# Kernel tuning notes

Hardware: AMD Instinct MI355X
Metric: run time of the kernel (lower is better)

## Reference

```python
import jax, jax.numpy as jnp
import numpy as np

EMBED = 1024
B, I, J = 8, 2048, 2048
SCALE = EMBED ** -0.5


def setup_inputs() -> dict:
    key = jax.random.key(0)
    ks = jax.random.split(key, 5)
    s = EMBED ** -0.5  # init scale for weights
    return {
        "q_in": jax.random.normal(ks[0], (B, I, EMBED), dtype=jnp.float32),
        "k_v": jax.random.normal(ks[1], (B, J, EMBED), dtype=jnp.float32),
        "Wq": jax.random.normal(ks[2], (EMBED, EMBED), dtype=jnp.float32) * s,
        "bq": jnp.zeros((EMBED,), dtype=jnp.float32),
        "Wk": jax.random.normal(ks[3], (EMBED, EMBED), dtype=jnp.float32) * s,
        "bk": jnp.zeros((EMBED,), dtype=jnp.float32),
        "Wv": jax.random.normal(ks[4], (EMBED, EMBED), dtype=jnp.float32) * s,
        "bv": jnp.zeros((EMBED,), dtype=jnp.float32),
    }


def reference(q_in, k_v, Wq, bq, Wk, bk, Wv, bv):
    # Linear projections (torch Linear: x @ W.T + b; here W stored as [in, out])
    q = q_in @ Wq + bq            # [b, i, d]
    k = k_v @ Wk + bk             # [b, j, d]
    v = k_v @ Wv + bv             # [b, j, d]
    sim = jnp.einsum('bid,bjd->bij', q, k) * SCALE  # [b, i, j]
    attn = jax.nn.softmax(sim, axis=-1)
    # dropout with drop_rate=0.0 is identity
    out = jnp.einsum('bij,bjd->bid', attn, v)       # [b, i, d]
    return out
```

## Files before the change

### kernel.cpp

```cpp
#include <hip/hip_runtime.h>
#include <hip/hip_bf16.h>


#define BATCH 8
#define SEQ   2048
#define EMB   1024
#define SC2   0.045084222f

typedef __attribute__((ext_vector_type(8))) short bf16x8;
typedef __attribute__((ext_vector_type(4))) float f32x4;
typedef __attribute__((ext_vector_type(4))) unsigned short u16x4;
typedef __attribute__((ext_vector_type(8))) unsigned short u16x8;
typedef __attribute__((ext_vector_type(4))) float fl4;

__device__ __forceinline__ unsigned short f2bf(float f) {
    unsigned u = __builtin_bit_cast(unsigned, f);
    unsigned r = u + 0x7fffu + ((u >> 16) & 1u);
    return (unsigned short)(r >> 16);
}
__device__ __forceinline__ float bf2f(unsigned short s) {
    return __builtin_bit_cast(float, ((unsigned)s) << 16);
}
__device__ __forceinline__ void gload16(const unsigned short* g, unsigned short* l) {
    __builtin_amdgcn_global_load_lds(
        (const __attribute__((address_space(1))) void*)g,
        (__attribute__((address_space(3))) void*)l, 16, 0, 0);
}

__global__ __launch_bounds__(256)
void convert_all(const float* __restrict__ q_in, const float* __restrict__ k_v,
                 const float* __restrict__ Wq, const float* __restrict__ Wk,
                 const float* __restrict__ Wv,
                 unsigned short* __restrict__ qbin, unsigned short* __restrict__ kvbin,
                 unsigned short* __restrict__ Wt)
{
    const int bid = blockIdx.x;
    const int tid = threadIdx.x;
    if (bid < 4096) {
        const size_t N = (size_t)BATCH * SEQ * EMB;
        size_t idx = ((size_t)bid * 256 + tid) * 8;
        const size_t stride = (size_t)4096 * 256 * 8;
        for (; idx < N; idx += stride) {
            fl4 a0 = *(const fl4*)&q_in[idx];
            fl4 a1 = *(const fl4*)&q_in[idx + 4];
            fl4 b0 = *(const fl4*)&k_v[idx];
            fl4 b1 = *(const fl4*)&k_v[idx + 4];
            u16x8 ua, ub;
#pragma unroll
            for (int i = 0; i < 4; i++) {
                ua[i] = f2bf(a0[i]); ua[i + 4] = f2bf(a1[i]);
                ub[i] = f2bf(b0[i]); ub[i + 4] = f2bf(b1[i]);
            }
            *(u16x8*)&qbin[idx] = ua;
            *(u16x8*)&kvbin[idx] = ub;
        }
    } else {
        const int b2 = bid - 4096;
        const int wsel = b2 >> 8, rest = b2 & 255;
        const float* W = (wsel == 0) ? Wq : (wsel == 1) ? Wk : Wv;
        unsigned short* O = Wt + (size_t)wsel * EMB * EMB;
        const int k0 = (rest >> 4) * 64;
        const int n0 = (rest & 15) * 64;
        __shared__ unsigned short l[64 * 65];
#pragma unroll
        for (int it = 0; it < 16; it++) {
            const int lin = it * 256 + tid;
            const int k = lin >> 6, n = lin & 63;
            l[n * 65 + k] = f2bf(W[(size_t)(k0 + k) * EMB + n0 + n]);
        }
        __syncthreads();
#pragma unroll
        for (int it = 0; it < 16; it++) {
            const int lin = it * 256 + tid;
            const int n = lin >> 6, k = lin & 63;
            O[(size_t)(n0 + n) * EMB + k0 + k] = l[n * 65 + k];
        }
    }
}

__device__ __forceinline__ void stageT(const unsigned short* lanebase, size_t rstride,
                                       unsigned short* lwave) {
#pragma unroll
    for (int i = 0; i < 2; i++)
        gload16(lanebase + (size_t)(i * 128) * rstride, lwave + i * 4096);
}

#define PIPE_TILE(SLOT, DO_STAGE, STAGE_A_BASE, STAGE_A_LDS, STAGE_B_BASE, STAGE_B_LDS) \
    {                                                                           \
        const unsigned short* pa = &sA[SLOT][0];                                \
        const unsigned short* pb = &sB[SLOT][0];                                \
        bf16x8 a0 = *(bf16x8*)&pa[aoff0];                                       \
        bf16x8 a1 = *(bf16x8*)&pa[aoff0 + 512];                                 \
        bf16x8 a2 = *(bf16x8*)&pa[aoff0 + 1024];                                \
        bf16x8 a3 = *(bf16x8*)&pa[aoff0 + 1536];                                \
        bf16x8 a4 = *(bf16x8*)&pa[aoff0 + 2048];                                \
        bf16x8 a5 = *(bf16x8*)&pa[aoff0 + 2560];                                \
        bf16x8 a6 = *(bf16x8*)&pa[aoff0 + 3072];                                \
        bf16x8 a7 = *(bf16x8*)&pa[aoff0 + 3584];                                \
        bf16x8 bv0 = *(bf16x8*)&pb[boff0];                                      \
        bf16x8 bv1 = *(bf16x8*)&pb[boff0 + 512];                                \
        bf16x8 bv2 = *(bf16x8*)&pb[boff0 + 1024];                               \
        bf16x8 bv3 = *(bf16x8*)&pb[boff0 + 1536];                               \
        if (DO_STAGE) stageT(STAGE_A_BASE, strideA, STAGE_A_LDS);               \
        __builtin_amdgcn_s_setprio(1);                                          \
        acc[0][0] = __builtin_amdgcn_mfma_f32_16x16x32_bf16(a0, bv0, acc[0][0], 0, 0, 0); \
        acc[0][1] = __builtin_amdgcn_mfma_f32_16x16x32_bf16(a0, bv1, acc[0][1], 0, 0, 0); \
        acc[0][2] = __builtin_amdgcn_mfma_f32_16x16x32_bf16(a0, bv2, acc[0][2], 0, 0, 0); \
        acc[0][3] = __builtin_amdgcn_mfma_f32_16x16x32_bf16(a0, bv3, acc[0][3], 0, 0, 0); \
        acc[1][0] = __builtin_amdgcn_mfma_f32_16x16x32_bf16(a1, bv0, acc[1][0], 0, 0, 0); \
        acc[1][1] = __builtin_amdgcn_mfma_f32_16x16x32_bf16(a1, bv1, acc[1][1], 0, 0, 0); \
        acc[1][2] = __builtin_amdgcn_mfma_f32_16x16x32_bf16(a1, bv2, acc[1][2], 0, 0, 0); \
        acc[1][3] = __builtin_amdgcn_mfma_f32_16x16x32_bf16(a1, bv3, acc[1][3], 0, 0, 0); \
        acc[2][0] = __builtin_amdgcn_mfma_f32_16x16x32_bf16(a2, bv0, acc[2][0], 0, 0, 0); \
        acc[2][1] = __builtin_amdgcn_mfma_f32_16x16x32_bf16(a2, bv1, acc[2][1], 0, 0, 0); \
        acc[2][2] = __builtin_amdgcn_mfma_f32_16x16x32_bf16(a2, bv2, acc[2][2], 0, 0, 0); \
        acc[2][3] = __builtin_amdgcn_mfma_f32_16x16x32_bf16(a2, bv3, acc[2][3], 0, 0, 0); \
        acc[3][0] = __builtin_amdgcn_mfma_f32_16x16x32_bf16(a3, bv0, acc[3][0], 0, 0, 0); \
        acc[3][1] = __builtin_amdgcn_mfma_f32_16x16x32_bf16(a3, bv1, acc[3][1], 0, 0, 0); \
        acc[3][2] = __builtin_amdgcn_mfma_f32_16x16x32_bf16(a3, bv2, acc[3][2], 0, 0, 0); \
        acc[3][3] = __builtin_amdgcn_mfma_f32_16x16x32_bf16(a3, bv3, acc[3][3], 0, 0, 0); \
        __builtin_amdgcn_s_setprio(0);                                          \
        if (DO_STAGE) stageT(STAGE_B_BASE, strideB, STAGE_B_LDS);               \
        __builtin_amdgcn_s_setprio(1);                                          \
        acc[4][0] = __builtin_amdgcn_mfma_f32_16x16x32_bf16(a4, bv0, acc[4][0], 0, 0, 0); \
        acc[4][1] = __builtin_amdgcn_mfma_f32_16x16x32_bf16(a4, bv1, acc[4][1], 0, 0, 0); \
        acc[4][2] = __builtin_amdgcn_mfma_f32_16x16x32_bf16(a4, bv2, acc[4][2], 0, 0, 0); \
        acc[4][3] = __builtin_amdgcn_mfma_f32_16x16x32_bf16(a4, bv3, acc[4][3], 0, 0, 0); \
        acc[5][0] = __builtin_amdgcn_mfma_f32_16x16x32_bf16(a5, bv0, acc[5][0], 0, 0, 0); \
        acc[5][1] = __builtin_amdgcn_mfma_f32_16x16x32_bf16(a5, bv1, acc[5][1], 0, 0, 0); \
        acc[5][2] = __builtin_amdgcn_mfma_f32_16x16x32_bf16(a5, bv2, acc[5][2], 0, 0, 0); \
        acc[5][3] = __builtin_amdgcn_mfma_f32_16x16x32_bf16(a5, bv3, acc[5][3], 0, 0, 0); \
        acc[6][0] = __builtin_amdgcn_mfma_f32_16x16x32_bf16(a6, bv0, acc[6][0], 0, 0, 0); \
        acc[6][1] = __builtin_amdgcn_mfma_f32_16x16x32_bf16(a6, bv1, acc[6][1], 0, 0, 0); \
        acc[6][2] = __builtin_amdgcn_mfma_f32_16x16x32_bf16(a6, bv2, acc[6][2], 0, 0, 0); \
        acc[6][3] = __builtin_amdgcn_mfma_f32_16x16x32_bf16(a6, bv3, acc[6][3], 0, 0, 0); \
        acc[7][0] = __builtin_amdgcn_mfma_f32_16x16x32_bf16(a7, bv0, acc[7][0], 0, 0, 0); \
        acc[7][1] = __builtin_amdgcn_mfma_f32_16x16x32_bf16(a7, bv1, acc[7][1], 0, 0, 0); \
        acc[7][2] = __builtin_amdgcn_mfma_f32_16x16x32_bf16(a7, bv2, acc[7][2], 0, 0, 0); \
        acc[7][3] = __builtin_amdgcn_mfma_f32_16x16x32_bf16(a7, bv3, acc[7][3], 0, 0, 0); \
        __builtin_amdgcn_s_setprio(0);                                          \
        asm volatile("s_waitcnt vmcnt(4)" ::: "memory");                        \
        __builtin_amdgcn_s_barrier();                                           \
        __builtin_amdgcn_sched_barrier(0);                                      \
    }

__device__ __forceinline__ void pipe_gemm(
    const unsigned short* __restrict__ Asrc,
    const unsigned short* __restrict__ Bsrc,
    const size_t strideA, const size_t strideB, const int NT,
    unsigned short (*sA)[8192], unsigned short (*sB)[8192],
    const int lwave, const int aoff0, const int boff0,
    f32x4 acc[8][4])
{
    stageT(Asrc, strideA, &sA[0][lwave]);
    stageT(Bsrc, strideB, &sB[0][lwave]);
    stageT(Asrc + 32, strideA, &sA[1][lwave]);
    stageT(Bsrc + 32, strideB, &sB[1][lwave]);
    asm volatile("s_waitcnt vmcnt(4)" ::: "memory");
    __builtin_amdgcn_s_barrier();
    __builtin_amdgcn_sched_barrier(0);

    for (int T = 0; T < NT; ++T) {
        const int s = T & 3;
        const int doStage = (T + 2 < NT);
        const int s2 = (T + 2) & 3;
        PIPE_TILE(s, doStage, Asrc + (T + 2) * 32, &sA[s2][lwave],
                  Bsrc + (T + 2) * 32, &sB[s2][lwave]);
    }
}

#define PIPE_PREAMBLE                                                     \
    __shared__ unsigned short sMem[65536];                    \
    unsigned short (*sA)[8192] = (unsigned short (*)[8192])sMem;          \
    unsigned short (*sB)[8192] = (unsigned short (*)[8192])(sMem + 32768);\
    const int tid = threadIdx.x, lane = tid & 63;                         \
    const int wid = tid >> 6, wr = wid >> 2, wn = wid & 3;                \
    const int r = lane & 15, g = lane >> 4;                               \
    const int lwave = (wid << 9);                                         \
    const int scol = ((tid & 3) ^ ((tid >> 3) & 3)) * 8;                  \
    const int gsw = (g ^ ((r >> 1) & 3)) * 8;                             \
    const int aoff0 = (wr * 128 + r) * 32 + gsw;                          \
    const int boff0 = (wn * 64 + r) * 32 + gsw;                           \
    f32x4 acc[8][4];                                                      \
    _Pragma("unroll") for (int i_ = 0; i_ < 8; i_++)                      \
    _Pragma("unroll") for (int j_ = 0; j_ < 4; j_++) acc[i_][j_] = (f32x4)0.0f;

__device__ __forceinline__ void lds_flush_bf16(const unsigned short* sP,
                                               unsigned short* gbase,
                                               size_t gstride, int tid)
{
    const int lane = tid & 63, wv = tid >> 6;
    const int rowsel = lane >> 5, jj = lane & 31;
#pragma unroll
    for (int it = 0; it < 16; ++it) {
        const int row = it * 16 + wv * 2 + rowsel;
        const int byte = row * 512 + ((jj * 16) ^ ((row & 7) << 4));
        u16x8 v = *(const u16x8*)((const char*)sP + byte);
        *(u16x8*)&gbase[(size_t)row * gstride + jj * 8] = v;
    }
}

__global__ __launch_bounds__(512, 1)
void proj_all(const unsigned short* __restrict__ Wt,
              const unsigned short* __restrict__ qbin,
              const unsigned short* __restrict__ kvbin,
              const float* __restrict__ bq, const float* __restrict__ bk,
              const float* __restrict__ bv,
              unsigned short* __restrict__ qb, unsigned short* __restrict__ kb,
              unsigned short* __restrict__ vt)
{
    PIPE_PREAMBLE
    const int bid = blockIdx.x;
    const size_t strideA = EMB, strideB = EMB;
    const unsigned short* Asrc;
    const unsigned short* Bsrc;
    int d0 = 0, i0 = 0, m0 = 0, n0 = 0;
    const bool qrole = (bid < 256);
    if (qrole) {
        const int lid = (bid & 7) * 32 + (bid >> 3);
        d0 = (lid & 3) * 256; i0 = (lid >> 2) * 256;
        Asrc = Wt + (size_t)(d0 + (tid >> 2)) * EMB + scol;
        Bsrc = qbin + (size_t)(i0 + (tid >> 2)) * EMB + scol;
    } else {
        const int b2 = bid - 256;
        const int lid = (b2 & 7) * 64 + (b2 >> 3);
        n0 = (lid & 7) * 256; m0 = (lid >> 3) * 256;
        Asrc = kvbin + (size_t)(m0 + (tid >> 2)) * EMB + scol;
        Bsrc = Wt + (size_t)EMB * EMB + (size_t)(n0 + (tid >> 2)) * EMB + scol;
    }

    pipe_gemm(Asrc, Bsrc, strideA, strideB, EMB / 32, sA, sB, lwave, aoff0, boff0, acc);

    if (qrole) {
#pragma unroll
        for (int mm = 0; mm < 8; mm++) {
            const int colb = wr * 128 + mm * 16 + g * 4;
            const fl4 b4 = *(const fl4*)&bq[d0 + colb];
#pragma unroll
            for (int n = 0; n < 4; n++) {
                const int row = wn * 64 + n * 16 + r;
                u16x4 u;
#pragma unroll
                for (int c = 0; c < 4; c++) u[c] = f2bf(acc[mm][n][c] + b4[c]);
                const int byte = row * 512 + ((colb * 2) ^ ((row & 7) << 4));
                *(u16x4*)((char*)sMem + byte) = u;
            }
        }
        __syncthreads();
        lds_flush_bf16(sMem, qb + (size_t)i0 * EMB + d0, EMB, tid);
    } else {
        const int b = m0 >> 11;
        const int j0l = m0 & 2047;
        if (n0 < 1024) {
#pragma unroll
            for (int mm = 0; mm < 8; mm++) {
                const int ibase = m0 + wr * 128 + mm * 16 + g * 4;
#pragma unroll
                for (int n = 0; n < 4; n++) {
                    const int col = n0 + wn * 64 + n * 16 + r;
                    const float bb = bk[col];
#pragma unroll
                    for (int c = 0; c < 4; c++)
                        kb[(size_t)(ibase + c) * EMB + col] = f2bf(acc[mm][n][c] + bb);
                }
            }
        } else {
#pragma unroll
            for (int mm = 0; mm < 8; mm++) {
                const int colb = wr * 128 + mm * 16 + g * 4;
#pragma unroll
                for (int n = 0; n < 4; n++) {
                    const int row = wn * 64 + n * 16 + r;
                    const float bb = bv[n0 - 1024 + row];
                    u16x4 u;
#pragma unroll
                    for (int c = 0; c < 4; c++) u[c] = f2bf(acc[mm][n][c] + bb);
                    const int byte = row * 512 + ((colb * 2) ^ ((row & 7) << 4));
                    *(u16x4*)((char*)sMem + byte) = u;
                }
            }
            __syncthreads();
            lds_flush_bf16(sMem, vt + ((size_t)b * EMB + (n0 - 1024)) * SEQ + j0l,
                           SEQ, tid);
        }
    }
}

__global__ __launch_bounds__(512, 1)
void qk256_kernel(const unsigned short* __restrict__ qb,
                  const unsigned short* __restrict__ kb,
                  unsigned short* __restrict__ P,
                  float* __restrict__ Ppart)
{
    PIPE_PREAMBLE
    const int bid = blockIdx.x;
    const int lid = (bid & 7) * 64 + (bid >> 3);
    const int b = lid >> 6, jt = (lid >> 3) & 7, it = lid & 7;
    const int j0 = jt * 256, i0 = it * 256;
    const size_t strideA = EMB, strideB = EMB;
    const unsigned short* Ag = kb + (size_t)b * SEQ * EMB;
    const unsigned short* Bg = qb + (size_t)b * SEQ * EMB;
    const unsigned short* Asrc = Ag + (size_t)(j0 + (tid >> 2)) * EMB + scol;
    const unsigned short* Bsrc = Bg + (size_t)(i0 + (tid >> 2)) * EMB + scol;

    pipe_gemm(Asrc, Bsrc, strideA, strideB, EMB / 32, sA, sB, lwave, aoff0, boff0, acc);

    float ps[4] = {0.f, 0.f, 0.f, 0.f};
#pragma unroll
    for (int mm = 0; mm < 8; mm++) {
        const int colb = wr * 128 + mm * 16 + g * 4;
#pragma unroll
        for (int n = 0; n < 4; n++) {
            const int row = wn * 64 + n * 16 + r;
            u16x4 u;
#pragma unroll
            for (int c = 0; c < 4; c++) {
                const float p = exp2f(acc[mm][n][c] * SC2);
                ps[n] += p;
                u[c] = f2bf(p);
            }
            const int byte = row * 512 + ((colb * 2) ^ ((row & 7) << 4));
            *(u16x4*)((char*)sMem + byte) = u;
        }
    }
#pragma unroll
    for (int n = 0; n < 4; n++) {
        ps[n] += __shfl_xor(ps[n], 16);
        ps[n] += __shfl_xor(ps[n], 32);
    }
    if (g == 0) {
        const int slot = jt * 2 + wr;
        float* pp = Ppart + (size_t)slot * (BATCH * SEQ) + (size_t)b * SEQ;
#pragma unroll
        for (int n = 0; n < 4; n++)
            pp[i0 + wn * 64 + n * 16 + r] = ps[n];
    }
    __syncthreads();
    unsigned short* Pb = P + (size_t)b * SEQ * SEQ;
    lds_flush_bf16(sMem, Pb + (size_t)i0 * SEQ + j0, SEQ, tid);
}

__global__ __launch_bounds__(512, 1)
void pv256_kernel(const unsigned short* __restrict__ P,
                  const unsigned short* __restrict__ vt,
                  const float* __restrict__ Ppart,
                  float* __restrict__ out)
{
    PIPE_PREAMBLE
    const int bid = blockIdx.x;
    const int lid = (bid & 7) * 32 + (bid >> 3);
    const int b = lid >> 5, it = (lid >> 2) & 7, dt = lid & 3;
    const int d0 = dt * 256, i0 = it * 256;
    const size_t strideA = SEQ, strideB = SEQ;
    const unsigned short* Ag = vt + (size_t)b * EMB * SEQ;
    const unsigned short* Bg = P + (size_t)b * SEQ * SEQ;
    const unsigned short* Asrc = Ag + (size_t)(d0 + (tid >> 2)) * SEQ + scol;
    const unsigned short* Bsrc = Bg + (size_t)(i0 + (tid >> 2)) * SEQ + scol;

    float inv[4];
#pragma unroll
    for (int n = 0; n < 4; n++) {
        const int row = b * SEQ + i0 + wn * 64 + n * 16 + r;
        float s = 0.f;
#pragma unroll
        for (int slot = 0; slot < 16; slot++)
            s += Ppart[(size_t)slot * (BATCH * SEQ) + row];
        inv[n] = 1.0f / s;
    }

    pipe_gemm(Asrc, Bsrc, strideA, strideB, SEQ / 32, sA, sB, lwave, aoff0, boff0, acc);

    float* ob = out + (size_t)b * SEQ * EMB;
    float* sF = (float*)sMem;
#pragma unroll
    for (int h = 0; h < 2; h++) {
        if (wr == h) {
#pragma unroll
            for (int mm = 0; mm < 8; mm++) {
                const int colb = mm * 16 + g * 4;
#pragma unroll
                for (int n = 0; n < 4; n++) {
                    const int row = wn * 64 + n * 16 + r;
                    fl4 o;
#pragma unroll
                    for (int c = 0; c < 4; c++) o[c] = acc[mm][n][c] * inv[n];
                    const int byte = row * 512 + ((colb * 4) ^ ((row & 7) << 4));
                    *(fl4*)((char*)sF + byte) = o;
                }
            }
        }
        __syncthreads();
        {
            const int rowsel = lane >> 5, jj = lane & 31;
#pragma unroll
            for (int itx = 0; itx < 16; ++itx) {
                const int row = itx * 16 + wid * 2 + rowsel;
                const int byte = row * 512 + ((jj * 16) ^ ((row & 7) << 4));
                fl4 v = *(const fl4*)((const char*)sF + byte);
                *(fl4*)&ob[(size_t)(i0 + row) * EMB + d0 + h * 128 + jj * 4] = v;
            }
        }
        if (h == 0) __syncthreads();
    }
}

extern "C" void kernel_launch(void* const* d_in, const int* in_sizes, int n_in,
                              void* d_out, int out_size, void* d_ws, size_t ws_size,
                              hipStream_t stream)
{
    const float* q_in = (const float*)d_in[0];
    const float* k_v  = (const float*)d_in[1];
    const float* Wq   = (const float*)d_in[2];
    const float* bq   = (const float*)d_in[3];
    const float* Wk   = (const float*)d_in[4];
    const float* bk   = (const float*)d_in[5];
    const float* Wv   = (const float*)d_in[6];
    const float* bv   = (const float*)d_in[7];
    float* out = (float*)d_out;

    char* ws = (char*)d_ws;
    unsigned short* qbin = (unsigned short*)(ws);
    unsigned short* kvbin= (unsigned short*)(ws + (size_t)33554432);
    unsigned short* P    = (unsigned short*)(ws);
    unsigned short* qb   = (unsigned short*)(ws + (size_t)67108864);
    unsigned short* kb   = (unsigned short*)(ws + (size_t)100663296);
    unsigned short* vt   = (unsigned short*)(ws + (size_t)134217728);
    unsigned short* Wt   = (unsigned short*)(ws + (size_t)167772160);
    float*          Ppart= (float*)(ws + (size_t)174063616);

    convert_all<<<4864, 256, 0, stream>>>(q_in, k_v, Wq, Wk, Wv, qbin, kvbin, Wt);
    proj_all<<<768, 512, 0, stream>>>(Wt, qbin, kvbin, bq, bk, bv, qb, kb, vt);
    qk256_kernel<<<512, 512, 0, stream>>>(qb, kb, P, Ppart);
    pv256_kernel<<<256, 512, 0, stream>>>(P, vt, Ppart, out);
}
```

Measured before the change: 293.9 us.

## Split GEMM main loop into barrier-synchronized half-phases with interleaved LDS reads

Adds a phased pipe_gemm variant in which each K-tile is split into two halves. Each half loads its A fragments from LDS, issues one global-to-LDS stage, hits a workgroup barrier and lgkmcnt wait, then runs 16 MFMAs, so waves stay in lockstep and LDS reads overlap more evenly with compute. The tail iterations now wait with vmcnt(0) when no new stage was issued. The QK and PV kernels switch to the new variant, which cuts register pressure for A fragments but adds extra barriers per tile.

Result: slower. 306.2 us (+4.2%).

```diff
diff --git a/kernel.cpp b/kernel.cpp
--- a/kernel.cpp
+++ b/kernel.cpp
@@ -85,64 +85,41 @@
         gload16(lanebase + (size_t)(i * 128) * rstride, lwave + i * 4096);
 }
 
-#define PIPE_TILE(SLOT, DO_STAGE, STAGE_A_BASE, STAGE_A_LDS, STAGE_B_BASE, STAGE_B_LDS) \
-    {                                                                           \
-        const unsigned short* pa = &sA[SLOT][0];                                \
-        const unsigned short* pb = &sB[SLOT][0];                                \
-        bf16x8 a0 = *(bf16x8*)&pa[aoff0];                                       \
-        bf16x8 a1 = *(bf16x8*)&pa[aoff0 + 512];                                 \
-        bf16x8 a2 = *(bf16x8*)&pa[aoff0 + 1024];                                \
-        bf16x8 a3 = *(bf16x8*)&pa[aoff0 + 1536];                                \
-        bf16x8 a4 = *(bf16x8*)&pa[aoff0 + 2048];                                \
-        bf16x8 a5 = *(bf16x8*)&pa[aoff0 + 2560];                                \
-        bf16x8 a6 = *(bf16x8*)&pa[aoff0 + 3072];                                \
-        bf16x8 a7 = *(bf16x8*)&pa[aoff0 + 3584];                                \
-        bf16x8 bv0 = *(bf16x8*)&pb[boff0];                                      \
-        bf16x8 bv1 = *(bf16x8*)&pb[boff0 + 512];                                \
-        bf16x8 bv2 = *(bf16x8*)&pb[boff0 + 1024];                               \
-        bf16x8 bv3 = *(bf16x8*)&pb[boff0 + 1536];                               \
-        if (DO_STAGE) stageT(STAGE_A_BASE, strideA, STAGE_A_LDS);               \
-        __builtin_amdgcn_s_setprio(1);                                          \
-        acc[0][0] = __builtin_amdgcn_mfma_f32_16x16x32_bf16(a0, bv0, acc[0][0], 0, 0, 0); \
-        acc[0][1] = __builtin_amdgcn_mfma_f32_16x16x32_bf16(a0, bv1, acc[0][1], 0, 0, 0); \
-        acc[0][2] = __builtin_amdgcn_mfma_f32_16x16x32_bf16(a0, bv2, acc[0][2], 0, 0, 0); \
-        acc[0][3] = __builtin_amdgcn_mfma_f32_16x16x32_bf16(a0, bv3, acc[0][3], 0, 0, 0); \
-        acc[1][0] = __builtin_amdgcn_mfma_f32_16x16x32_bf16(a1, bv0, acc[1][0], 0, 0, 0); \
-        acc[1][1] = __builtin_amdgcn_mfma_f32_16x16x32_bf16(a1, bv1, acc[1][1], 0, 0, 0); \
-        acc[1][2] = __builtin_amdgcn_mfma_f32_16x16x32_bf16(a1, bv2, acc[1][2], 0, 0, 0); \
-        acc[1][3] = __builtin_amdgcn_mfma_f32_16x16x32_bf16(a1, bv3, acc[1][3], 0, 0, 0); \
-        acc[2][0] = __builtin_amdgcn_mfma_f32_16x16x32_bf16(a2, bv0, acc[2][0], 0, 0, 0); \
-        acc[2][1] = __builtin_amdgcn_mfma_f32_16x16x32_bf16(a2, bv1, acc[2][1], 0, 0, 0); \
-        acc[2][2] = __builtin_amdgcn_mfma_f32_16x16x32_bf16(a2, bv2, acc[2][2], 0, 0, 0); \
-        acc[2][3] = __builtin_amdgcn_mfma_f32_16x16x32_bf16(a2, bv3, acc[2][3], 0, 0, 0); \
-        acc[3][0] = __builtin_amdgcn_mfma_f32_16x16x32_bf16(a3, bv0, acc[3][0], 0, 0, 0); \
-        acc[3][1] = __builtin_amdgcn_mfma_f32_16x16x32_bf16(a3, bv1, acc[3][1], 0, 0, 0); \
-        acc[3][2] = __builtin_amdgcn_mfma_f32_16x16x32_bf16(a3, bv2, acc[3][2], 0, 0, 0); \
-        acc[3][3] = __builtin_amdgcn_mfma_f32_16x16x32_bf16(a3, bv3, acc[3][3], 0, 0, 0); \
-        __builtin_amdgcn_s_setprio(0);                                          \
-        if (DO_STAGE) stageT(STAGE_B_BASE, strideB, STAGE_B_LDS);               \
-        __builtin_amdgcn_s_setprio(1);                                          \
-        acc[4][0] = __builtin_amdgcn_mfma_f32_16x16x32_bf16(a4, bv0, acc[4][0], 0, 0, 0); \
-        acc[4][1] = __builtin_amdgcn_mfma_f32_16x16x32_bf16(a4, bv1, acc[4][1], 0, 0, 0); \
-        acc[4][2] = __builtin_amdgcn_mfma_f32_16x16x32_bf16(a4, bv2, acc[4][2], 0, 0, 0); \
-        acc[4][3] = __builtin_amdgcn_mfma_f32_16x16x32_bf16(a4, bv3, acc[4][3], 0, 0, 0); \
-        acc[5][0] = __builtin_amdgcn_mfma_f32_16x16x32_bf16(a5, bv0, acc[5][0], 0, 0, 0); \
-        acc[5][1] = __builtin_amdgcn_mfma_f32_16x16x32_bf16(a5, bv1, acc[5][1], 0, 0, 0); \
-        acc[5][2] = __builtin_amdgcn_mfma_f32_16x16x32_bf16(a5, bv2, acc[5][2], 0, 0, 0); \
-        acc[5][3] = __builtin_amdgcn_mfma_f32_16x16x32_bf16(a5, bv3, acc[5][3], 0, 0, 0); \
-        acc[6][0] = __builtin_amdgcn_mfma_f32_16x16x32_bf16(a6, bv0, acc[6][0], 0, 0, 0); \
-        acc[6][1] = __builtin_amdgcn_mfma_f32_16x16x32_bf16(a6, bv1, acc[6][1], 0, 0, 0); \
-        acc[6][2] = __builtin_amdgcn_mfma_f32_16x16x32_bf16(a6, bv2, acc[6][2], 0, 0, 0); \
-        acc[6][3] = __builtin_amdgcn_mfma_f32_16x16x32_bf16(a6, bv3, acc[6][3], 0, 0, 0); \
-        acc[7][0] = __builtin_amdgcn_mfma_f32_16x16x32_bf16(a7, bv0, acc[7][0], 0, 0, 0); \
-        acc[7][1] = __builtin_amdgcn_mfma_f32_16x16x32_bf16(a7, bv1, acc[7][1], 0, 0, 0); \
-        acc[7][2] = __builtin_amdgcn_mfma_f32_16x16x32_bf16(a7, bv2, acc[7][2], 0, 0, 0); \
-        acc[7][3] = __builtin_amdgcn_mfma_f32_16x16x32_bf16(a7, bv3, acc[7][3], 0, 0, 0); \
-        __builtin_amdgcn_s_setprio(0);                                          \
-        asm volatile("s_waitcnt vmcnt(4)" ::: "memory");                        \
-        __builtin_amdgcn_s_barrier();                                           \
-        __builtin_amdgcn_sched_barrier(0);                                      \
-    }
+#define MFMA16_LO(A0,A1,A2,A3)                                                  \
+        acc[0][0] = __builtin_amdgcn_mfma_f32_16x16x32_bf16(A0, bv0, acc[0][0], 0, 0, 0); \
+        acc[0][1] = __builtin_amdgcn_mfma_f32_16x16x32_bf16(A0, bv1, acc[0][1], 0, 0, 0); \
+        acc[0][2] = __builtin_amdgcn_mfma_f32_16x16x32_bf16(A0, bv2, acc[0][2], 0, 0, 0); \
+        acc[0][3] = __builtin_amdgcn_mfma_f32_16x16x32_bf16(A0, bv3, acc[0][3], 0, 0, 0); \
+        acc[1][0] = __builtin_amdgcn_mfma_f32_16x16x32_bf16(A1, bv0, acc[1][0], 0, 0, 0); \
+        acc[1][1] = __builtin_amdgcn_mfma_f32_16x16x32_bf16(A1, bv1, acc[1][1], 0, 0, 0); \
+        acc[1][2] = __builtin_amdgcn_mfma_f32_16x16x32_bf16(A1, bv2, acc[1][2], 0, 0, 0); \
+        acc[1][3] = __builtin_amdgcn_mfma_f32_16x16x32_bf16(A1, bv3, acc[1][3], 0, 0, 0); \
+        acc[2][0] = __builtin_amdgcn_mfma_f32_16x16x32_bf16(A2, bv0, acc[2][0], 0, 0, 0); \
+        acc[2][1] = __builtin_amdgcn_mfma_f32_16x16x32_bf16(A2, bv1, acc[2][1], 0, 0, 0); \
+        acc[2][2] = __builtin_amdgcn_mfma_f32_16x16x32_bf16(A2, bv2, acc[2][2], 0, 0, 0); \
+        acc[2][3] = __builtin_amdgcn_mfma_f32_16x16x32_bf16(A2, bv3, acc[2][3], 0, 0, 0); \
+        acc[3][0] = __builtin_amdgcn_mfma_f32_16x16x32_bf16(A3, bv0, acc[3][0], 0, 0, 0); \
+        acc[3][1] = __builtin_amdgcn_mfma_f32_16x16x32_bf16(A3, bv1, acc[3][1], 0, 0, 0); \
+        acc[3][2] = __builtin_amdgcn_mfma_f32_16x16x32_bf16(A3, bv2, acc[3][2], 0, 0, 0); \
+        acc[3][3] = __builtin_amdgcn_mfma_f32_16x16x32_bf16(A3, bv3, acc[3][3], 0, 0, 0);
+
+#define MFMA16_HI(A4,A5,A6,A7)                                                  \
+        acc[4][0] = __builtin_amdgcn_mfma_f32_16x16x32_bf16(A4, bv0, acc[4][0], 0, 0, 0); \
+        acc[4][1] = __builtin_amdgcn_mfma_f32_16x16x32_bf16(A4, bv1, acc[4][1], 0, 0, 0); \
+        acc[4][2] = __builtin_amdgcn_mfma_f32_16x16x32_bf16(A4, bv2, acc[4][2], 0, 0, 0); \
+        acc[4][3] = __builtin_amdgcn_mfma_f32_16x16x32_bf16(A4, bv3, acc[4][3], 0, 0, 0); \
+        acc[5][0] = __builtin_amdgcn_mfma_f32_16x16x32_bf16(A5, bv0, acc[5][0], 0, 0, 0); \
+        acc[5][1] = __builtin_amdgcn_mfma_f32_16x16x32_bf16(A5, bv1, acc[5][1], 0, 0, 0); \
+        acc[5][2] = __builtin_amdgcn_mfma_f32_16x16x32_bf16(A5, bv2, acc[5][2], 0, 0, 0); \
+        acc[5][3] = __builtin_amdgcn_mfma_f32_16x16x32_bf16(A5, bv3, acc[5][3], 0, 0, 0); \
+        acc[6][0] = __builtin_amdgcn_mfma_f32_16x16x32_bf16(A6, bv0, acc[6][0], 0, 0, 0); \
+        acc[6][1] = __builtin_amdgcn_mfma_f32_16x16x32_bf16(A6, bv1, acc[6][1], 0, 0, 0); \
+        acc[6][2] = __builtin_amdgcn_mfma_f32_16x16x32_bf16(A6, bv2, acc[6][2], 0, 0, 0); \
+        acc[6][3] = __builtin_amdgcn_mfma_f32_16x16x32_bf16(A6, bv3, acc[6][3], 0, 0, 0); \
+        acc[7][0] = __builtin_amdgcn_mfma_f32_16x16x32_bf16(A7, bv0, acc[7][0], 0, 0, 0); \
+        acc[7][1] = __builtin_amdgcn_mfma_f32_16x16x32_bf16(A7, bv1, acc[7][1], 0, 0, 0); \
+        acc[7][2] = __builtin_amdgcn_mfma_f32_16x16x32_bf16(A7, bv2, acc[7][2], 0, 0, 0); \
+        acc[7][3] = __builtin_amdgcn_mfma_f32_16x16x32_bf16(A7, bv3, acc[7][3], 0, 0, 0);
 
 __device__ __forceinline__ void pipe_gemm(
     const unsigned short* __restrict__ Asrc,
@@ -164,8 +141,89 @@
         const int s = T & 3;
         const int doStage = (T + 2 < NT);
         const int s2 = (T + 2) & 3;
-        PIPE_TILE(s, doStage, Asrc + (T + 2) * 32, &sA[s2][lwave],
-                  Bsrc + (T + 2) * 32, &sB[s2][lwave]);
+        const unsigned short* pa = &sA[s][0];
+        const unsigned short* pb = &sB[s][0];
+        bf16x8 a0 = *(bf16x8*)&pa[aoff0];
+        bf16x8 a1 = *(bf16x8*)&pa[aoff0 + 512];
+        bf16x8 a2 = *(bf16x8*)&pa[aoff0 + 1024];
+        bf16x8 a3 = *(bf16x8*)&pa[aoff0 + 1536];
+        bf16x8 a4 = *(bf16x8*)&pa[aoff0 + 2048];
+        bf16x8 a5 = *(bf16x8*)&pa[aoff0 + 2560];
+        bf16x8 a6 = *(bf16x8*)&pa[aoff0 + 3072];
+        bf16x8 a7 = *(bf16x8*)&pa[aoff0 + 3584];
+        bf16x8 bv0 = *(bf16x8*)&pb[boff0];
+        bf16x8 bv1 = *(bf16x8*)&pb[boff0 + 512];
+        bf16x8 bv2 = *(bf16x8*)&pb[boff0 + 1024];
+        bf16x8 bv3 = *(bf16x8*)&pb[boff0 + 1536];
+        if (doStage) stageT(Asrc + (T + 2) * 32, strideA, &sA[s2][lwave]);
+        __builtin_amdgcn_s_setprio(1);
+        MFMA16_LO(a0, a1, a2, a3)
+        __builtin_amdgcn_s_setprio(0);
+        if (doStage) stageT(Bsrc + (T + 2) * 32, strideB, &sB[s2][lwave]);
+        __builtin_amdgcn_s_setprio(1);
+        MFMA16_HI(a4, a5, a6, a7)
+        __builtin_amdgcn_s_setprio(0);
+        if (doStage) { asm volatile("s_waitcnt vmcnt(4)" ::: "memory"); }
+        else         { asm volatile("s_waitcnt vmcnt(0)" ::: "memory"); }
+        __builtin_amdgcn_s_barrier();
+        __builtin_amdgcn_sched_barrier(0);
+    }
+}
+
+__device__ __forceinline__ void pipe_gemm_ph(
+    const unsigned short* __restrict__ Asrc,
+    const unsigned short* __restrict__ Bsrc,
+    const size_t strideA, const size_t strideB, const int NT,
+    unsigned short (*sA)[8192], unsigned short (*sB)[8192],
+    const int lwave, const int aoff0, const int boff0,
+    f32x4 acc[8][4])
+{
+    stageT(Asrc, strideA, &sA[0][lwave]);
+    stageT(Bsrc, strideB, &sB[0][lwave]);
+    stageT(Asrc + 32, strideA, &sA[1][lwave]);
+    stageT(Bsrc + 32, strideB, &sB[1][lwave]);
+    asm volatile("s_waitcnt vmcnt(4)" ::: "memory");
+    __builtin_amdgcn_s_barrier();
+    __builtin_amdgcn_sched_barrier(0);
+
+    for (int T = 0; T < NT; ++T) {
+        const int s = T & 3;
+        const int doStage = (T + 2 < NT);
+        const int s2 = (T + 2) & 3;
+        const unsigned short* pa = &sA[s][0];
+        const unsigned short* pb = &sB[s][0];
+        bf16x8 a0 = *(bf16x8*)&pa[aoff0];
+        bf16x8 a1 = *(bf16x8*)&pa[aoff0 + 512];
+        bf16x8 a2 = *(bf16x8*)&pa[aoff0 + 1024];
+        bf16x8 a3 = *(bf16x8*)&pa[aoff0 + 1536];
+        bf16x8 bv0 = *(bf16x8*)&pb[boff0];
+        bf16x8 bv1 = *(bf16x8*)&pb[boff0 + 512];
+        bf16x8 bv2 = *(bf16x8*)&pb[boff0 + 1024];
+        bf16x8 bv3 = *(bf16x8*)&pb[boff0 + 1536];
+        if (doStage) stageT(Asrc + (T + 2) * 32, strideA, &sA[s2][lwave]);
+        __builtin_amdgcn_s_barrier();
+        asm volatile("s_waitcnt lgkmcnt(0)" ::: "memory");
+        __builtin_amdgcn_sched_barrier(0);
+        __builtin_amdgcn_s_setprio(1);
+        MFMA16_LO(a0, a1, a2, a3)
+        __builtin_amdgcn_s_setprio(0);
+        __builtin_amdgcn_s_barrier();
+        __builtin_amdgcn_sched_barrier(0);
+        bf16x8 a4 = *(bf16x8*)&pa[aoff0 + 2048];
+        bf16x8 a5 = *(bf16x8*)&pa[aoff0 + 2560];
+        bf16x8 a6 = *(bf16x8*)&pa[aoff0 + 3072];
+        bf16x8 a7 = *(bf16x8*)&pa[aoff0 + 3584];
+        if (doStage) stageT(Bsrc + (T + 2) * 32, strideB, &sB[s2][lwave]);
+        __builtin_amdgcn_s_barrier();
+        asm volatile("s_waitcnt lgkmcnt(0)" ::: "memory");
+        __builtin_amdgcn_sched_barrier(0);
+        __builtin_amdgcn_s_setprio(1);
+        MFMA16_HI(a4, a5, a6, a7)
+        __builtin_amdgcn_s_setprio(0);
+        if (doStage) { asm volatile("s_waitcnt vmcnt(4)" ::: "memory"); }
+        else         { asm volatile("s_waitcnt vmcnt(0)" ::: "memory"); }
+        __builtin_amdgcn_s_barrier();
+        __builtin_amdgcn_sched_barrier(0);
     }
 }
 
@@ -303,7 +361,7 @@
     const unsigned short* Asrc = Ag + (size_t)(j0 + (tid >> 2)) * EMB + scol;
     const unsigned short* Bsrc = Bg + (size_t)(i0 + (tid >> 2)) * EMB + scol;
 
-    pipe_gemm(Asrc, Bsrc, strideA, strideB, EMB / 32, sA, sB, lwave, aoff0, boff0, acc);
+    pipe_gemm_ph(Asrc, Bsrc, strideA, strideB, EMB / 32, sA, sB, lwave, aoff0, boff0, acc);
 
     float ps[4] = {0.f, 0.f, 0.f, 0.f};
 #pragma unroll
@@ -368,7 +426,7 @@
         inv[n] = 1.0f / s;
     }
 
-    pipe_gemm(Asrc, Bsrc, strideA, strideB, SEQ / 32, sA, sB, lwave, aoff0, boff0, acc);
+    pipe_gemm_ph(Asrc, Bsrc, strideA, strideB, SEQ / 32, sA, sB, lwave, aoff0, boff0, acc);
 
     float* ob = out + (size_t)b * SEQ * EMB;
     float* sF = (float*)sMem;
```

## Switch GEMM pipeline to double-buffered 64-wide K tiles with 8-way swizzle

Applied to the files above, without the earlier changes.

Replaces the 4-slot, 32-wide-K LDS ring (prefetch distance two) with two 64-wide K buffers (prefetch distance one). Each iteration now does two MFMA groups, so barriers and waitcnts are halved. The LDS swizzle and global staging indexing widen from 4 to 8 chunks. In exchange, vmcnt(0) forces each prefetch to finish within a single iteration, which leaves less latency slack than the previous deeper pipeline.

Result: no change. 289.1 us, median of 2 (-1.6%).

```diff
diff --git a/kernel.cpp b/kernel.cpp
--- a/kernel.cpp
+++ b/kernel.cpp
@@ -78,109 +78,124 @@
     }
 }
 
-__device__ __forceinline__ void stageT(const unsigned short* lanebase, size_t rstride,
-                                       unsigned short* lwave) {
-#pragma unroll
-    for (int i = 0; i < 2; i++)
-        gload16(lanebase + (size_t)(i * 128) * rstride, lwave + i * 4096);
-}
-
-#define PIPE_TILE(SLOT, DO_STAGE, STAGE_A_BASE, STAGE_A_LDS, STAGE_B_BASE, STAGE_B_LDS) \
-    {                                                                           \
-        const unsigned short* pa = &sA[SLOT][0];                                \
-        const unsigned short* pb = &sB[SLOT][0];                                \
-        bf16x8 a0 = *(bf16x8*)&pa[aoff0];                                       \
-        bf16x8 a1 = *(bf16x8*)&pa[aoff0 + 512];                                 \
-        bf16x8 a2 = *(bf16x8*)&pa[aoff0 + 1024];                                \
-        bf16x8 a3 = *(bf16x8*)&pa[aoff0 + 1536];                                \
-        bf16x8 a4 = *(bf16x8*)&pa[aoff0 + 2048];                                \
-        bf16x8 a5 = *(bf16x8*)&pa[aoff0 + 2560];                                \
-        bf16x8 a6 = *(bf16x8*)&pa[aoff0 + 3072];                                \
-        bf16x8 a7 = *(bf16x8*)&pa[aoff0 + 3584];                                \
-        bf16x8 bv0 = *(bf16x8*)&pb[boff0];                                      \
-        bf16x8 bv1 = *(bf16x8*)&pb[boff0 + 512];                                \
-        bf16x8 bv2 = *(bf16x8*)&pb[boff0 + 1024];                               \
-        bf16x8 bv3 = *(bf16x8*)&pb[boff0 + 1536];                               \
-        if (DO_STAGE) stageT(STAGE_A_BASE, strideA, STAGE_A_LDS);               \
-        __builtin_amdgcn_s_setprio(1);                                          \
-        acc[0][0] = __builtin_amdgcn_mfma_f32_16x16x32_bf16(a0, bv0, acc[0][0], 0, 0, 0); \
-        acc[0][1] = __builtin_amdgcn_mfma_f32_16x16x32_bf16(a0, bv1, acc[0][1], 0, 0, 0); \
-        acc[0][2] = __builtin_amdgcn_mfma_f32_16x16x32_bf16(a0, bv2, acc[0][2], 0, 0, 0); \
-        acc[0][3] = __builtin_amdgcn_mfma_f32_16x16x32_bf16(a0, bv3, acc[0][3], 0, 0, 0); \
-        acc[1][0] = __builtin_amdgcn_mfma_f32_16x16x32_bf16(a1, bv0, acc[1][0], 0, 0, 0); \
-        acc[1][1] = __builtin_amdgcn_mfma_f32_16x16x32_bf16(a1, bv1, acc[1][1], 0, 0, 0); \
-        acc[1][2] = __builtin_amdgcn_mfma_f32_16x16x32_bf16(a1, bv2, acc[1][2], 0, 0, 0); \
-        acc[1][3] = __builtin_amdgcn_mfma_f32_16x16x32_bf16(a1, bv3, acc[1][3], 0, 0, 0); \
-        acc[2][0] = __builtin_amdgcn_mfma_f32_16x16x32_bf16(a2, bv0, acc[2][0], 0, 0, 0); \
-        acc[2][1] = __builtin_amdgcn_mfma_f32_16x16x32_bf16(a2, bv1, acc[2][1], 0, 0, 0); \
-        acc[2][2] = __builtin_amdgcn_mfma_f32_16x16x32_bf16(a2, bv2, acc[2][2], 0, 0, 0); \
-        acc[2][3] = __builtin_amdgcn_mfma_f32_16x16x32_bf16(a2, bv3, acc[2][3], 0, 0, 0); \
-        acc[3][0] = __builtin_amdgcn_mfma_f32_16x16x32_bf16(a3, bv0, acc[3][0], 0, 0, 0); \
-        acc[3][1] = __builtin_amdgcn_mfma_f32_16x16x32_bf16(a3, bv1, acc[3][1], 0, 0, 0); \
-        acc[3][2] = __builtin_amdgcn_mfma_f32_16x16x32_bf16(a3, bv2, acc[3][2], 0, 0, 0); \
-        acc[3][3] = __builtin_amdgcn_mfma_f32_16x16x32_bf16(a3, bv3, acc[3][3], 0, 0, 0); \
-        __builtin_amdgcn_s_setprio(0);                                          \
-        if (DO_STAGE) stageT(STAGE_B_BASE, strideB, STAGE_B_LDS);               \
-        __builtin_amdgcn_s_setprio(1);                                          \
-        acc[4][0] = __builtin_amdgcn_mfma_f32_16x16x32_bf16(a4, bv0, acc[4][0], 0, 0, 0); \
-        acc[4][1] = __builtin_amdgcn_mfma_f32_16x16x32_bf16(a4, bv1, acc[4][1], 0, 0, 0); \
-        acc[4][2] = __builtin_amdgcn_mfma_f32_16x16x32_bf16(a4, bv2, acc[4][2], 0, 0, 0); \
-        acc[4][3] = __builtin_amdgcn_mfma_f32_16x16x32_bf16(a4, bv3, acc[4][3], 0, 0, 0); \
-        acc[5][0] = __builtin_amdgcn_mfma_f32_16x16x32_bf16(a5, bv0, acc[5][0], 0, 0, 0); \
-        acc[5][1] = __builtin_amdgcn_mfma_f32_16x16x32_bf16(a5, bv1, acc[5][1], 0, 0, 0); \
-        acc[5][2] = __builtin_amdgcn_mfma_f32_16x16x32_bf16(a5, bv2, acc[5][2], 0, 0, 0); \
-        acc[5][3] = __builtin_amdgcn_mfma_f32_16x16x32_bf16(a5, bv3, acc[5][3], 0, 0, 0); \
-        acc[6][0] = __builtin_amdgcn_mfma_f32_16x16x32_bf16(a6, bv0, acc[6][0], 0, 0, 0); \
-        acc[6][1] = __builtin_amdgcn_mfma_f32_16x16x32_bf16(a6, bv1, acc[6][1], 0, 0, 0); \
-        acc[6][2] = __builtin_amdgcn_mfma_f32_16x16x32_bf16(a6, bv2, acc[6][2], 0, 0, 0); \
-        acc[6][3] = __builtin_amdgcn_mfma_f32_16x16x32_bf16(a6, bv3, acc[6][3], 0, 0, 0); \
-        acc[7][0] = __builtin_amdgcn_mfma_f32_16x16x32_bf16(a7, bv0, acc[7][0], 0, 0, 0); \
-        acc[7][1] = __builtin_amdgcn_mfma_f32_16x16x32_bf16(a7, bv1, acc[7][1], 0, 0, 0); \
-        acc[7][2] = __builtin_amdgcn_mfma_f32_16x16x32_bf16(a7, bv2, acc[7][2], 0, 0, 0); \
-        acc[7][3] = __builtin_amdgcn_mfma_f32_16x16x32_bf16(a7, bv3, acc[7][3], 0, 0, 0); \
-        __builtin_amdgcn_s_setprio(0);                                          \
-        asm volatile("s_waitcnt vmcnt(4)" ::: "memory");                        \
-        __builtin_amdgcn_s_barrier();                                           \
-        __builtin_amdgcn_sched_barrier(0);                                      \
-    }
+__device__ __forceinline__ void stage64(const unsigned short* lanebase, size_t rstride,
+                                        unsigned short* lbuf) {
+#pragma unroll
+    for (int i = 0; i < 4; i++)
+        gload16(lanebase + (size_t)(i * 64) * rstride, lbuf + i * 4096);
+}
+
+#define MFMA32(A0,A1,A2,A3,A4,A5,A6,A7,B0,B1,B2,B3)                             \
+        acc[0][0] = __builtin_amdgcn_mfma_f32_16x16x32_bf16(A0, B0, acc[0][0], 0, 0, 0); \
+        acc[0][1] = __builtin_amdgcn_mfma_f32_16x16x32_bf16(A0, B1, acc[0][1], 0, 0, 0); \
+        acc[0][2] = __builtin_amdgcn_mfma_f32_16x16x32_bf16(A0, B2, acc[0][2], 0, 0, 0); \
+        acc[0][3] = __builtin_amdgcn_mfma_f32_16x16x32_bf16(A0, B3, acc[0][3], 0, 0, 0); \
+        acc[1][0] = __builtin_amdgcn_mfma_f32_16x16x32_bf16(A1, B0, acc[1][0], 0, 0, 0); \
+        acc[1][1] = __builtin_amdgcn_mfma_f32_16x16x32_bf16(A1, B1, acc[1][1], 0, 0, 0); \
+        acc[1][2] = __builtin_amdgcn_mfma_f32_16x16x32_bf16(A1, B2, acc[1][2], 0, 0, 0); \
+        acc[1][3] = __builtin_amdgcn_mfma_f32_16x16x32_bf16(A1, B3, acc[1][3], 0, 0, 0); \
+        acc[2][0] = __builtin_amdgcn_mfma_f32_16x16x32_bf16(A2, B0, acc[2][0], 0, 0, 0); \
+        acc[2][1] = __builtin_amdgcn_mfma_f32_16x16x32_bf16(A2, B1, acc[2][1], 0, 0, 0); \
+        acc[2][2] = __builtin_amdgcn_mfma_f32_16x16x32_bf16(A2, B2, acc[2][2], 0, 0, 0); \
+        acc[2][3] = __builtin_amdgcn_mfma_f32_16x16x32_bf16(A2, B3, acc[2][3], 0, 0, 0); \
+        acc[3][0] = __builtin_amdgcn_mfma_f32_16x16x32_bf16(A3, B0, acc[3][0], 0, 0, 0); \
+        acc[3][1] = __builtin_amdgcn_mfma_f32_16x16x32_bf16(A3, B1, acc[3][1], 0, 0, 0); \
+        acc[3][2] = __builtin_amdgcn_mfma_f32_16x16x32_bf16(A3, B2, acc[3][2], 0, 0, 0); \
+        acc[3][3] = __builtin_amdgcn_mfma_f32_16x16x32_bf16(A3, B3, acc[3][3], 0, 0, 0); \
+        acc[4][0] = __builtin_amdgcn_mfma_f32_16x16x32_bf16(A4, B0, acc[4][0], 0, 0, 0); \
+        acc[4][1] = __builtin_amdgcn_mfma_f32_16x16x32_bf16(A4, B1, acc[4][1], 0, 0, 0); \
+        acc[4][2] = __builtin_amdgcn_mfma_f32_16x16x32_bf16(A4, B2, acc[4][2], 0, 0, 0); \
+        acc[4][3] = __builtin_amdgcn_mfma_f32_16x16x32_bf16(A4, B3, acc[4][3], 0, 0, 0); \
+        acc[5][0] = __builtin_amdgcn_mfma_f32_16x16x32_bf16(A5, B0, acc[5][0], 0, 0, 0); \
+        acc[5][1] = __builtin_amdgcn_mfma_f32_16x16x32_bf16(A5, B1, acc[5][1], 0, 0, 0); \
+        acc[5][2] = __builtin_amdgcn_mfma_f32_16x16x32_bf16(A5, B2, acc[5][2], 0, 0, 0); \
+        acc[5][3] = __builtin_amdgcn_mfma_f32_16x16x32_bf16(A5, B3, acc[5][3], 0, 0, 0); \
+        acc[6][0] = __builtin_amdgcn_mfma_f32_16x16x32_bf16(A6, B0, acc[6][0], 0, 0, 0); \
+        acc[6][1] = __builtin_amdgcn_mfma_f32_16x16x32_bf16(A6, B1, acc[6][1], 0, 0, 0); \
+        acc[6][2] = __builtin_amdgcn_mfma_f32_16x16x32_bf16(A6, B2, acc[6][2], 0, 0, 0); \
+        acc[6][3] = __builtin_amdgcn_mfma_f32_16x16x32_bf16(A6, B3, acc[6][3], 0, 0, 0); \
+        acc[7][0] = __builtin_amdgcn_mfma_f32_16x16x32_bf16(A7, B0, acc[7][0], 0, 0, 0); \
+        acc[7][1] = __builtin_amdgcn_mfma_f32_16x16x32_bf16(A7, B1, acc[7][1], 0, 0, 0); \
+        acc[7][2] = __builtin_amdgcn_mfma_f32_16x16x32_bf16(A7, B2, acc[7][2], 0, 0, 0); \
+        acc[7][3] = __builtin_amdgcn_mfma_f32_16x16x32_bf16(A7, B3, acc[7][3], 0, 0, 0);
 
 __device__ __forceinline__ void pipe_gemm(
     const unsigned short* __restrict__ Asrc,
     const unsigned short* __restrict__ Bsrc,
     const size_t strideA, const size_t strideB, const int NT,
-    unsigned short (*sA)[8192], unsigned short (*sB)[8192],
-    const int lwave, const int aoff0, const int boff0,
+    unsigned short (*sA)[16384], unsigned short (*sB)[16384],
+    const int lwave, const int abase, const int bbase,
+    const int swk0, const int swk1,
     f32x4 acc[8][4])
 {
-    stageT(Asrc, strideA, &sA[0][lwave]);
-    stageT(Bsrc, strideB, &sB[0][lwave]);
-    stageT(Asrc + 32, strideA, &sA[1][lwave]);
-    stageT(Bsrc + 32, strideB, &sB[1][lwave]);
-    asm volatile("s_waitcnt vmcnt(4)" ::: "memory");
+    stage64(Asrc, strideA, &sA[0][lwave]);
+    stage64(Bsrc, strideB, &sB[0][lwave]);
+    asm volatile("s_waitcnt vmcnt(0)" ::: "memory");
     __builtin_amdgcn_s_barrier();
     __builtin_amdgcn_sched_barrier(0);
 
     for (int T = 0; T < NT; ++T) {
-        const int s = T & 3;
-        const int doStage = (T + 2 < NT);
-        const int s2 = (T + 2) & 3;
-        PIPE_TILE(s, doStage, Asrc + (T + 2) * 32, &sA[s2][lwave],
-                  Bsrc + (T + 2) * 32, &sB[s2][lwave]);
+        const int cur = T & 1, nxt = cur ^ 1;
+        const int doStage = (T + 1 < NT);
+        const unsigned short* pa = &sA[cur][0];
+        const unsigned short* pb = &sB[cur][0];
+        {
+            bf16x8 a0 = *(bf16x8*)&pa[abase + swk0];
+            bf16x8 a1 = *(bf16x8*)&pa[abase + 1024 + swk0];
+            bf16x8 a2 = *(bf16x8*)&pa[abase + 2048 + swk0];
+            bf16x8 a3 = *(bf16x8*)&pa[abase + 3072 + swk0];
+            bf16x8 a4 = *(bf16x8*)&pa[abase + 4096 + swk0];
+            bf16x8 a5 = *(bf16x8*)&pa[abase + 5120 + swk0];
+            bf16x8 a6 = *(bf16x8*)&pa[abase + 6144 + swk0];
+            bf16x8 a7 = *(bf16x8*)&pa[abase + 7168 + swk0];
+            bf16x8 bv0 = *(bf16x8*)&pb[bbase + swk0];
+            bf16x8 bv1 = *(bf16x8*)&pb[bbase + 1024 + swk0];
+            bf16x8 bv2 = *(bf16x8*)&pb[bbase + 2048 + swk0];
+            bf16x8 bv3 = *(bf16x8*)&pb[bbase + 3072 + swk0];
+            if (doStage) {
+                stage64(Asrc + (T + 1) * 64, strideA, &sA[nxt][lwave]);
+                stage64(Bsrc + (T + 1) * 64, strideB, &sB[nxt][lwave]);
+            }
+            __builtin_amdgcn_s_setprio(1);
+            MFMA32(a0, a1, a2, a3, a4, a5, a6, a7, bv0, bv1, bv2, bv3)
+            __builtin_amdgcn_s_setprio(0);
+        }
+        {
+            bf16x8 a0 = *(bf16x8*)&pa[abase + swk1];
+            bf16x8 a1 = *(bf16x8*)&pa[abase + 1024 + swk1];
+            bf16x8 a2 = *(bf16x8*)&pa[abase + 2048 + swk1];
+            bf16x8 a3 = *(bf16x8*)&pa[abase + 3072 + swk1];
+            bf16x8 a4 = *(bf16x8*)&pa[abase + 4096 + swk1];
+            bf16x8 a5 = *(bf16x8*)&pa[abase + 5120 + swk1];
+            bf16x8 a6 = *(bf16x8*)&pa[abase + 6144 + swk1];
+            bf16x8 a7 = *(bf16x8*)&pa[abase + 7168 + swk1];
+            bf16x8 bv0 = *(bf16x8*)&pb[bbase + swk1];
+            bf16x8 bv1 = *(bf16x8*)&pb[bbase + 1024 + swk1];
+            bf16x8 bv2 = *(bf16x8*)&pb[bbase + 2048 + swk1];
+            bf16x8 bv3 = *(bf16x8*)&pb[bbase + 3072 + swk1];
+            __builtin_amdgcn_s_setprio(1);
+            MFMA32(a0, a1, a2, a3, a4, a5, a6, a7, bv0, bv1, bv2, bv3)
+            __builtin_amdgcn_s_setprio(0);
+        }
+        asm volatile("s_waitcnt vmcnt(0)" ::: "memory");
+        __builtin_amdgcn_s_barrier();
+        __builtin_amdgcn_sched_barrier(0);
     }
 }
 
 #define PIPE_PREAMBLE                                                     \
     __shared__ unsigned short sMem[65536];                    \
-    unsigned short (*sA)[8192] = (unsigned short (*)[8192])sMem;          \
-    unsigned short (*sB)[8192] = (unsigned short (*)[8192])(sMem + 32768);\
+    unsigned short (*sA)[16384] = (unsigned short (*)[16384])sMem;        \
+    unsigned short (*sB)[16384] = (unsigned short (*)[16384])(sMem + 32768);\
     const int tid = threadIdx.x, lane = tid & 63;                         \
     const int wid = tid >> 6, wr = wid >> 2, wn = wid & 3;                \
     const int r = lane & 15, g = lane >> 4;                               \
     const int lwave = (wid << 9);                                         \
-    const int scol = ((tid & 3) ^ ((tid >> 3) & 3)) * 8;                  \
-    const int gsw = (g ^ ((r >> 1) & 3)) * 8;                             \
-    const int aoff0 = (wr * 128 + r) * 32 + gsw;                          \
-    const int boff0 = (wn * 64 + r) * 32 + gsw;                           \
+    const int scol = ((tid & 7) ^ ((tid >> 3) & 7)) * 8;                  \
+    const int swk0 = ((g) ^ (r & 7)) * 8;                                 \
+    const int swk1 = ((4 + g) ^ (r & 7)) * 8;                             \
+    const int abase = (wr * 128 + r) * 64;                                \
+    const int bbase = (wn * 64 + r) * 64;                                 \
     f32x4 acc[8][4];                                                      \
     _Pragma("unroll") for (int i_ = 0; i_ < 8; i_++)                      \
     _Pragma("unroll") for (int j_ = 0; j_ < 4; j_++) acc[i_][j_] = (f32x4)0.0f;
@@ -219,17 +234,18 @@
     if (qrole) {
         const int lid = (bid & 7) * 32 + (bid >> 3);
         d0 = (lid & 3) * 256; i0 = (lid >> 2) * 256;
-        Asrc = Wt + (size_t)(d0 + (tid >> 2)) * EMB + scol;
-        Bsrc = qbin + (size_t)(i0 + (tid >> 2)) * EMB + scol;
+        Asrc = Wt + (size_t)(d0 + (tid >> 3)) * EMB + scol;
+        Bsrc = qbin + (size_t)(i0 + (tid >> 3)) * EMB + scol;
     } else {
         const int b2 = bid - 256;
         const int lid = (b2 & 7) * 64 + (b2 >> 3);
         n0 = (lid & 7) * 256; m0 = (lid >> 3) * 256;
-        Asrc = kvbin + (size_t)(m0 + (tid >> 2)) * EMB + scol;
-        Bsrc = Wt + (size_t)EMB * EMB + (size_t)(n0 + (tid >> 2)) * EMB + scol;
-    }
-
-    pipe_gemm(Asrc, Bsrc, strideA, strideB, EMB / 32, sA, sB, lwave, aoff0, boff0, acc);
+        Asrc = kvbin + (size_t)(m0 + (tid >> 3)) * EMB + scol;
+        Bsrc = Wt + (size_t)EMB * EMB + (size_t)(n0 + (tid >> 3)) * EMB + scol;
+    }
+
+    pipe_gemm(Asrc, Bsrc, strideA, strideB, EMB / 64, sA, sB, lwave,
+              abase, bbase, swk0, swk1, acc);
 
     if (qrole) {
 #pragma unroll
@@ -300,10 +316,11 @@
     const size_t strideA = EMB, strideB = EMB;
     const unsigned short* Ag = kb + (size_t)b * SEQ * EMB;
     const unsigned short* Bg = qb + (size_t)b * SEQ * EMB;
-    const unsigned short* Asrc = Ag + (size_t)(j0 + (tid >> 2)) * EMB + scol;
-    const unsigned short* Bsrc = Bg + (size_t)(i0 + (tid >> 2)) * EMB + scol;
-
-    pipe_gemm(Asrc, Bsrc, strideA, strideB, EMB / 32, sA, sB, lwave, aoff0, boff0, acc);
+    const unsigned short* Asrc = Ag + (size_t)(j0 + (tid >> 3)) * EMB + scol;
+    const unsigned short* Bsrc = Bg + (size_t)(i0 + (tid >> 3)) * EMB + scol;
+
+    pipe_gemm(Asrc, Bsrc, strideA, strideB, EMB / 64, sA, sB, lwave,
+              abase, bbase, swk0, swk1, acc);
 
     float ps[4] = {0.f, 0.f, 0.f, 0.f};
 #pragma unroll
@@ -354,8 +371,8 @@
     const size_t strideA = SEQ, strideB = SEQ;
     const unsigned short* Ag = vt + (size_t)b * EMB * SEQ;
     const unsigned short* Bg = P + (size_t)b * SEQ * SEQ;
-    const unsigned short* Asrc = Ag + (size_t)(d0 + (tid >> 2)) * SEQ + scol;
-    const unsigned short* Bsrc = Bg + (size_t)(i0 + (tid >> 2)) * SEQ + scol;
+    const unsigned short* Asrc = Ag + (size_t)(d0 + (tid >> 3)) * SEQ + scol;
+    const unsigned short* Bsrc = Bg + (size_t)(i0 + (tid >> 3)) * SEQ + scol;
 
     float inv[4];
 #pragma unroll
@@ -368,7 +385,8 @@
         inv[n] = 1.0f / s;
     }
 
-    pipe_gemm(Asrc, Bsrc, strideA, strideB, SEQ / 32, sA, sB, lwave, aoff0, boff0, acc);
+    pipe_gemm(Asrc, Bsrc, strideA, strideB, SEQ / 64, sA, sB, lwave,
+              abase, bbase, swk0, swk1, acc);
 
     float* ob = out + (size_t)b * SEQ * EMB;
     float* sF = (float*)sMem;
```
